# Kernel tuning notes

Hardware: AMD Instinct MI355X
Metric: run time of the kernel (lower is better)

## Reference

```python
import jax, jax.numpy as jnp
import numpy as np

D_IN = 1024
D_OUT = 1024

def setup_inputs() -> dict:
    key = jax.random.key(0)
    kx, kq, kk, kv = jax.random.split(key, 4)
    x = jax.random.normal(kx, (4, 2048, D_IN), dtype=jnp.float32)
    # torch Linear weights are [d_out, d_in]; store as [d_in, d_out] for x @ W
    s = 1.0 / np.sqrt(D_IN)
    Wq = jax.random.uniform(kq, (D_IN, D_OUT), jnp.float32, -s, s)
    Wk = jax.random.uniform(kk, (D_IN, D_OUT), jnp.float32, -s, s)
    Wv = jax.random.uniform(kv, (D_IN, D_OUT), jnp.float32, -s, s)
    return {"x": x, "Wq": Wq, "Wk": Wk, "Wv": Wv}

def reference(x, Wq, Wk, Wv):
    # x: [b, n, d_in]
    n = x.shape[1]
    q = jnp.einsum('bnd,de->bne', x, Wq)
    k = jnp.einsum('bnd,de->bne', x, Wk)
    v = jnp.einsum('bnd,de->bne', x, Wv)
    scores = jnp.einsum('bqe,bke->bqk', q, k)  # [b, n, n]
    causal = jnp.tril(jnp.ones((n, n), dtype=bool))  # True = keep
    scores = jnp.where(causal, scores, -jnp.inf)
    attn = jax.nn.softmax(scores / jnp.sqrt(jnp.float32(k.shape[-1])), axis=-1)
    # dropout p=0.0 -> identity
    return jnp.einsum('bqk,bke->bqe', attn, v)
```

## Files before the change

kernel.cpp:

```cpp
#include <hip/hip_runtime.h>
#include <hip/hip_bf16.h>
#include <stdint.h>

#define D_ 1024
#define NSEQ 2048

typedef __attribute__((ext_vector_type(8))) short bf16x8;
typedef __attribute__((ext_vector_type(4))) float f32x4;

static __device__ __forceinline__ unsigned short f2bf(float x) {
    union { __hip_bfloat16 h; unsigned short u; } cv;
    cv.h = __float2bfloat16(x);
    return cv.u;
}

static __device__ __forceinline__ void gload_lds16(const void* g, void* l) {
    __builtin_amdgcn_global_load_lds(
        (const __attribute__((address_space(1))) unsigned int*)(uintptr_t)g,
        (__attribute__((address_space(3))) unsigned int*)(uintptr_t)l, 16, 0, 0);
}

__global__ __launch_bounds__(256) void cvt_x(const float* __restrict__ x,
                                             __hip_bfloat16* __restrict__ xb) {
    int i = blockIdx.x * 256 + threadIdx.x;
    float4 v = reinterpret_cast<const float4*>(x)[i];
    ushort4 o;
    o.x = f2bf(v.x); o.y = f2bf(v.y); o.z = f2bf(v.z); o.w = f2bf(v.w);
    reinterpret_cast<ushort4*>(xb)[i] = o;
}

__global__ __launch_bounds__(256) void wt_kernel(const float* __restrict__ Wq,
                                                 const float* __restrict__ Wk,
                                                 const float* __restrict__ Wv,
                                                 __hip_bfloat16* __restrict__ Wt) {
    const float* W = (blockIdx.z == 0) ? Wq : (blockIdx.z == 1) ? Wk : Wv;
    unsigned short* O = (unsigned short*)(Wt + (size_t)blockIdx.z * D_ * D_);
    __shared__ float tile[32][33];
    int r0 = blockIdx.y * 32, c0 = blockIdx.x * 32;
    int t = threadIdx.x;
    int r = t >> 3, c4 = (t & 7) * 4;
    float4 v = *reinterpret_cast<const float4*>(&W[(size_t)(r0 + r) * D_ + c0 + c4]);
    tile[r][c4 + 0] = v.x; tile[r][c4 + 1] = v.y;
    tile[r][c4 + 2] = v.z; tile[r][c4 + 3] = v.w;
    __syncthreads();
    int er = t >> 3, dc = (t & 7) * 4;
    ushort4 pk;
    pk.x = f2bf(tile[dc + 0][er]); pk.y = f2bf(tile[dc + 1][er]);
    pk.z = f2bf(tile[dc + 2][er]); pk.w = f2bf(tile[dc + 3][er]);
    *reinterpret_cast<ushort4*>(&O[(size_t)(c0 + er) * D_ + r0 + dc]) = pk;
}

template <int MODE>
__global__ __launch_bounds__(256) void gemm128(const __hip_bfloat16* __restrict__ A, int lda,
                                               const __hip_bfloat16* __restrict__ Bt, int ldb,
                                               void* __restrict__ o0, void* __restrict__ o1,
                                               void* __restrict__ o2,
                                               const float* __restrict__ rinv) {
    const int bx = blockIdx.x, by = blockIdx.y, bz = blockIdx.z;
    if (MODE == 2 && by > bx) return;

    const __hip_bfloat16* Ab = A;
    const __hip_bfloat16* Bb = Bt;
    int Kdim = 1024;
    if (MODE == 2) { Ab += (size_t)bz * NSEQ * D_;  Bb += (size_t)bz * NSEQ * D_; }
    if (MODE == 3) { Ab += (size_t)bz * NSEQ * 4096; Bb += (size_t)bz * D_ * NSEQ; Kdim = (bx + 1) * 128; }

    const int m0 = bx * 128, n0 = by * 128;

    __shared__ __hip_bfloat16 As[128 * 32];
    __shared__ __hip_bfloat16 Bs[128 * 32];

    const int tid = threadIdx.x;
    const int lane = tid & 63, wid = tid >> 6;
    const int wm = wid >> 1, wn = wid & 1;
    const int lr = lane & 15, lk = lane >> 4;

    const int srow = wid * 32 + (lane >> 2);
    const int scol = (lane & 3) * 8;
    const __hip_bfloat16* aptr = Ab + (size_t)(m0 + srow) * lda + scol;
    const __hip_bfloat16* bptr = Bb + (size_t)(n0 + srow) * ldb + scol;
    char* AsW = (char*)As + wid * 2048;
    char* BsW = (char*)Bs + wid * 2048;

    f32x4 acc[4][4] = {};

    for (int k0 = 0; k0 < Kdim; k0 += 32) {
        gload_lds16(aptr,                    AsW);
        gload_lds16(aptr + (size_t)16 * lda, AsW + 1024);
        gload_lds16(bptr,                    BsW);
        gload_lds16(bptr + (size_t)16 * ldb, BsW + 1024);
        aptr += 32; bptr += 32;
        __syncthreads();

        bf16x8 af[4], bfr[4];
#pragma unroll
        for (int m = 0; m < 4; ++m)
            af[m] = *reinterpret_cast<const bf16x8*>(&As[(wm * 64 + m * 16 + lr) * 32 + lk * 8]);
#pragma unroll
        for (int n = 0; n < 4; ++n)
            bfr[n] = *reinterpret_cast<const bf16x8*>(&Bs[(wn * 64 + n * 16 + lr) * 32 + lk * 8]);
#pragma unroll
        for (int m = 0; m < 4; ++m)
#pragma unroll
            for (int n = 0; n < 4; ++n)
                acc[m][n] = __builtin_amdgcn_mfma_f32_16x16x32_bf16(af[m], bfr[n], acc[m][n], 0, 0, 0);
        __syncthreads();
    }

#pragma unroll
    for (int m = 0; m < 4; ++m)
#pragma unroll
        for (int n = 0; n < 4; ++n) {
            const int rbase = m0 + wm * 64 + m * 16 + lk * 4;
            const int cbase = n0 + wn * 64 + n * 16 + lr;
            if (MODE == 0) {
                const int seg = cbase >> 10, e = cbase & 1023;
                if (seg < 2) {
                    unsigned short* C = (unsigned short*)(seg == 0 ? o0 : o1);
#pragma unroll
                    for (int j = 0; j < 4; ++j)
                        C[(size_t)(rbase + j) * D_ + e] = f2bf(acc[m][n][j]);
                } else {
                    unsigned short* Vt = (unsigned short*)o2;
                    const int b = rbase >> 11, nq = rbase & 2047;
                    ushort4 pk;
                    pk.x = f2bf(acc[m][n][0]); pk.y = f2bf(acc[m][n][1]);
                    pk.z = f2bf(acc[m][n][2]); pk.w = f2bf(acc[m][n][3]);
                    *reinterpret_cast<ushort4*>(&Vt[(((size_t)b << 10) + e) * NSEQ + nq]) = pk;
                }
            } else if (MODE == 2) {
                float* S = (float*)o0 + (size_t)bz * NSEQ * NSEQ;
#pragma unroll
                for (int j = 0; j < 4; ++j) {
                    const int qg = rbase + j, kg = cbase;
                    float s = acc[m][n][j] * 0.03125f;
                    if (kg > qg) s = -1e30f;
                    S[(size_t)qg * NSEQ + kg] = s;
                }
            } else if (MODE == 3) {
                float* O = (float*)o0 + (size_t)bz * NSEQ * D_;
#pragma unroll
                for (int j = 0; j < 4; ++j)
                    O[(size_t)(rbase + j) * D_ + cbase] =
                        acc[m][n][j] * rinv[bz * NSEQ + rbase + j];
            }
        }
}

__global__ __launch_bounds__(256) void softmax_rows(float* __restrict__ S,
                                                    float* __restrict__ rinv) {
    int lane = threadIdx.x & 63;
    int row = blockIdx.x * 4 + (threadIdx.x >> 6);
    int q = row & 2047;
    float* srow = S + (size_t)row * NSEQ;
    int L = ((q >> 7) + 1) << 7;

    float mx = -1e30f;
    for (int k = lane * 4; k < L; k += 256) {
        float4 v = *reinterpret_cast<const float4*>(srow + k);
        mx = fmaxf(mx, fmaxf(fmaxf(v.x, v.y), fmaxf(v.z, v.w)));
    }
    for (int off = 32; off > 0; off >>= 1) mx = fmaxf(mx, __shfl_xor(mx, off, 64));

    float sum = 0.f;
    unsigned short* prow = (unsigned short*)srow;
    for (int k = lane * 4; k < L; k += 256) {
        float4 v = *reinterpret_cast<const float4*>(srow + k);
        float e0 = __expf(v.x - mx), e1 = __expf(v.y - mx);
        float e2 = __expf(v.z - mx), e3 = __expf(v.w - mx);
        sum += (e0 + e1) + (e2 + e3);
        ushort4 pk; pk.x = f2bf(e0); pk.y = f2bf(e1); pk.z = f2bf(e2); pk.w = f2bf(e3);
        *reinterpret_cast<ushort4*>(prow + k) = pk;
    }
    for (int off = 32; off > 0; off >>= 1) sum += __shfl_xor(sum, off, 64);
    if (lane == 0) rinv[row] = 1.0f / sum;
}

extern "C" void kernel_launch(void* const* d_in, const int* in_sizes, int n_in,
                              void* d_out, int out_size, void* d_ws, size_t ws_size,
                              hipStream_t stream) {
    const float* x  = (const float*)d_in[0];
    const float* Wq = (const float*)d_in[1];
    const float* Wk = (const float*)d_in[2];
    const float* Wv = (const float*)d_in[3];

    char* ws = (char*)d_ws;
    float*          S    = (float*)(ws);
    __hip_bfloat16* Xb   = (__hip_bfloat16*)(ws + 67108864);
    __hip_bfloat16* Q    = (__hip_bfloat16*)(ws + 83886080);
    __hip_bfloat16* K    = (__hip_bfloat16*)(ws + 100663296);
    __hip_bfloat16* Vt   = (__hip_bfloat16*)(ws + 117440512);
    __hip_bfloat16* Wt   = (__hip_bfloat16*)(ws + 134217728);
    float*          rinv = (float*)(ws + 140509184);

    cvt_x<<<8192, 256, 0, stream>>>(x, Xb);
    wt_kernel<<<dim3(32, 32, 3), 256, 0, stream>>>(Wq, Wk, Wv, Wt);

    gemm128<0><<<dim3(64, 24, 1), 256, 0, stream>>>(Xb, 1024, Wt, 1024, Q, K, Vt, nullptr);
    gemm128<2><<<dim3(16, 16, 4), 256, 0, stream>>>(Q, 1024, K, 1024, S, nullptr, nullptr, nullptr);
    softmax_rows<<<2048, 256, 0, stream>>>(S, rinv);
    gemm128<3><<<dim3(16, 8, 4), 256, 0, stream>>>((const __hip_bfloat16*)S, 4096, Vt, 2048,
                                                   d_out, nullptr, nullptr, rinv);
}
```

Baseline: 193.1 us.

## Replace QKV projection GEMM with 256x256 tile, double-buffered, swizzled LDS pipeline

The fused QKV projection moves from the generic 128x128 single-buffered GEMM to a dedicated 512-thread kernel. It computes 256x256 output tiles and double-buffers a 128 KB LDS region with XOR-swizzled layout. Global-to-LDS loads for the next k-slab are issued while MFMAs run on the current one, using explicit vmcnt waits, barriers and setprio. The aim is to hide global load latency, reduce LDS bank conflicts and raise arithmetic intensity. The cost is heavy LDS use, which limits occupancy, and the 384-block grid may fill the CUs unevenly.

```diff
diff --git a/kernel.cpp b/kernel.cpp
--- a/kernel.cpp
+++ b/kernel.cpp
@@ -50,11 +50,172 @@
     *reinterpret_cast<ushort4*>(&O[(size_t)(c0 + er) * D_ + r0 + dc]) = pk;
 }
 
+
+struct Frags { bf16x8 a0, a1, a2, a3, b0, b1, b2, b3; };
+
+template <int KK, int MH>
+static __device__ __forceinline__ Frags load_frags(const char* bufbase, int aoff, int boff) {
+    const char* regA = bufbase + KK * 16384;
+    const char* regB = bufbase + 32768 + KK * 16384;
+    Frags f;
+    f.a0 = *(const bf16x8*)(regA + aoff + (MH * 4 + 0) * 1024);
+    f.a1 = *(const bf16x8*)(regA + aoff + (MH * 4 + 1) * 1024);
+    f.a2 = *(const bf16x8*)(regA + aoff + (MH * 4 + 2) * 1024);
+    f.a3 = *(const bf16x8*)(regA + aoff + (MH * 4 + 3) * 1024);
+    f.b0 = *(const bf16x8*)(regB + boff + 0);
+    f.b1 = *(const bf16x8*)(regB + boff + 1024);
+    f.b2 = *(const bf16x8*)(regB + boff + 2048);
+    f.b3 = *(const bf16x8*)(regB + boff + 3072);
+    return f;
+}
+
+template <int MH>
+static __device__ __forceinline__ void apply_mfma(const Frags& f, f32x4 (&acc)[8][4]) {
+    acc[MH*4+0][0] = __builtin_amdgcn_mfma_f32_16x16x32_bf16(f.a0, f.b0, acc[MH*4+0][0], 0, 0, 0);
+    acc[MH*4+0][1] = __builtin_amdgcn_mfma_f32_16x16x32_bf16(f.a0, f.b1, acc[MH*4+0][1], 0, 0, 0);
+    acc[MH*4+0][2] = __builtin_amdgcn_mfma_f32_16x16x32_bf16(f.a0, f.b2, acc[MH*4+0][2], 0, 0, 0);
+    acc[MH*4+0][3] = __builtin_amdgcn_mfma_f32_16x16x32_bf16(f.a0, f.b3, acc[MH*4+0][3], 0, 0, 0);
+    acc[MH*4+1][0] = __builtin_amdgcn_mfma_f32_16x16x32_bf16(f.a1, f.b0, acc[MH*4+1][0], 0, 0, 0);
+    acc[MH*4+1][1] = __builtin_amdgcn_mfma_f32_16x16x32_bf16(f.a1, f.b1, acc[MH*4+1][1], 0, 0, 0);
+    acc[MH*4+1][2] = __builtin_amdgcn_mfma_f32_16x16x32_bf16(f.a1, f.b2, acc[MH*4+1][2], 0, 0, 0);
+    acc[MH*4+1][3] = __builtin_amdgcn_mfma_f32_16x16x32_bf16(f.a1, f.b3, acc[MH*4+1][3], 0, 0, 0);
+    acc[MH*4+2][0] = __builtin_amdgcn_mfma_f32_16x16x32_bf16(f.a2, f.b0, acc[MH*4+2][0], 0, 0, 0);
+    acc[MH*4+2][1] = __builtin_amdgcn_mfma_f32_16x16x32_bf16(f.a2, f.b1, acc[MH*4+2][1], 0, 0, 0);
+    acc[MH*4+2][2] = __builtin_amdgcn_mfma_f32_16x16x32_bf16(f.a2, f.b2, acc[MH*4+2][2], 0, 0, 0);
+    acc[MH*4+2][3] = __builtin_amdgcn_mfma_f32_16x16x32_bf16(f.a2, f.b3, acc[MH*4+2][3], 0, 0, 0);
+    acc[MH*4+3][0] = __builtin_amdgcn_mfma_f32_16x16x32_bf16(f.a3, f.b0, acc[MH*4+3][0], 0, 0, 0);
+    acc[MH*4+3][1] = __builtin_amdgcn_mfma_f32_16x16x32_bf16(f.a3, f.b1, acc[MH*4+3][1], 0, 0, 0);
+    acc[MH*4+3][2] = __builtin_amdgcn_mfma_f32_16x16x32_bf16(f.a3, f.b2, acc[MH*4+3][2], 0, 0, 0);
+    acc[MH*4+3][3] = __builtin_amdgcn_mfma_f32_16x16x32_bf16(f.a3, f.b3, acc[MH*4+3][3], 0, 0, 0);
+}
+
+__global__ __launch_bounds__(512, 2) void gemm256_qkv(
+    const __hip_bfloat16* __restrict__ A,
+    const __hip_bfloat16* __restrict__ Bt,
+    void* __restrict__ q_out, void* __restrict__ k_out, void* __restrict__ vt_out) {
+    constexpr int NT = 16;
+    extern __shared__ char lds[];
+
+    const int m0 = blockIdx.x * 256, n0 = blockIdx.y * 256;
+    const int tid = threadIdx.x, lane = tid & 63, wid = tid >> 6;
+    const int wm = wid >> 2, wn = wid & 3;
+    const int lr = lane & 15, lk = lane >> 4;
+
+    const __hip_bfloat16* Apan = A + (size_t)m0 * 1024;
+    const __hip_bfloat16* Bpan = Bt + (size_t)n0 * 1024;
+
+    const int swz = (lk ^ ((lr >> 1) & 3)) << 4;
+    const int aoff = (wm * 128 + lr) * 64 + swz;
+    const int boff = (wn * 64 + lr) * 64 + swz;
+
+    const int sprow = wid * 32 + (lane >> 2);
+    const int sblk = ((lane & 3) ^ ((lane >> 3) & 3)) * 8;
+
+    auto stage = [&](int s) {
+        const int Ts = s >> 2, op = s & 1, kks = (s >> 1) & 1;
+        char* dst = lds + ((Ts & 1) << 16) + (op << 15) + (kks << 14) + (wid << 11);
+        const __hip_bfloat16* g = (op ? Bpan : Apan)
+                                  + (size_t)sprow * 1024 + Ts * 64 + kks * 32 + sblk;
+        gload_lds16(g, dst);
+        gload_lds16(g + (size_t)16 * 1024, dst + 1024);
+    };
+
+    f32x4 acc[8][4] = {};
+
+    stage(0); stage(1); stage(2); stage(3); stage(4);
+    asm volatile("s_waitcnt vmcnt(6)" ::: "memory");
+    __builtin_amdgcn_s_barrier();
+
+    for (int t = 0; t + 2 < NT; ++t) {
+        const char* bb = lds + ((t & 1) << 16);
+        const int s0 = 4 * t + 5;
+        {
+            Frags f = load_frags<0, 0>(bb, aoff, boff);
+            stage(s0 + 0);
+            __builtin_amdgcn_s_barrier();
+            asm volatile("s_waitcnt lgkmcnt(0)" ::: "memory");
+            __builtin_amdgcn_sched_barrier(0);
+            __builtin_amdgcn_s_setprio(1);
+            apply_mfma<0>(f, acc);
+            __builtin_amdgcn_s_setprio(0);
+            __builtin_amdgcn_s_barrier();
+        }
+        {
+            Frags f = load_frags<0, 1>(bb, aoff, boff);
+            stage(s0 + 1);
+            asm volatile("s_waitcnt vmcnt(6)" ::: "memory");
+            __builtin_amdgcn_s_barrier();
+            asm volatile("s_waitcnt lgkmcnt(0)" ::: "memory");
+            __builtin_amdgcn_sched_barrier(0);
+            __builtin_amdgcn_s_setprio(1);
+            apply_mfma<1>(f, acc);
+            __builtin_amdgcn_s_setprio(0);
+            __builtin_amdgcn_s_barrier();
+        }
+        {
+            Frags f = load_frags<1, 0>(bb, aoff, boff);
+            stage(s0 + 2);
+            __builtin_amdgcn_s_barrier();
+            asm volatile("s_waitcnt lgkmcnt(0)" ::: "memory");
+            __builtin_amdgcn_sched_barrier(0);
+            __builtin_amdgcn_s_setprio(1);
+            apply_mfma<0>(f, acc);
+            __builtin_amdgcn_s_setprio(0);
+            __builtin_amdgcn_s_barrier();
+        }
+        {
+            Frags f = load_frags<1, 1>(bb, aoff, boff);
+            stage(s0 + 3);
+            asm volatile("s_waitcnt vmcnt(6)" ::: "memory");
+            __builtin_amdgcn_s_barrier();
+            asm volatile("s_waitcnt lgkmcnt(0)" ::: "memory");
+            __builtin_amdgcn_sched_barrier(0);
+            __builtin_amdgcn_s_setprio(1);
+            apply_mfma<1>(f, acc);
+            __builtin_amdgcn_s_setprio(0);
+            __builtin_amdgcn_s_barrier();
+        }
+    }
+
+    stage(4 * NT - 3); stage(4 * NT - 2); stage(4 * NT - 1);
+    asm volatile("s_waitcnt vmcnt(0)" ::: "memory");
+    __builtin_amdgcn_s_barrier();
+#pragma unroll
+    for (int t = NT - 2; t < NT; ++t) {
+        const char* bb = lds + ((t & 1) << 16);
+        { Frags f = load_frags<0, 0>(bb, aoff, boff); apply_mfma<0>(f, acc); }
+        { Frags f = load_frags<0, 1>(bb, aoff, boff); apply_mfma<1>(f, acc); }
+        { Frags f = load_frags<1, 0>(bb, aoff, boff); apply_mfma<0>(f, acc); }
+        { Frags f = load_frags<1, 1>(bb, aoff, boff); apply_mfma<1>(f, acc); }
+    }
+
+#pragma unroll
+    for (int m = 0; m < 8; ++m)
+#pragma unroll
+        for (int n = 0; n < 4; ++n) {
+            const int rbase = m0 + wm * 128 + m * 16 + lk * 4;
+            const int cbase = n0 + wn * 64 + n * 16 + lr;
+            const int seg = cbase >> 10, e = cbase & 1023;
+            if (seg < 2) {
+                unsigned short* C = (unsigned short*)(seg == 0 ? q_out : k_out);
+#pragma unroll
+                for (int j = 0; j < 4; ++j)
+                    C[(size_t)(rbase + j) * D_ + e] = f2bf(acc[m][n][j]);
+            } else {
+                unsigned short* Vt = (unsigned short*)vt_out;
+                const int b = rbase >> 11, nq = rbase & 2047;
+                ushort4 pk;
+                pk.x = f2bf(acc[m][n][0]); pk.y = f2bf(acc[m][n][1]);
+                pk.z = f2bf(acc[m][n][2]); pk.w = f2bf(acc[m][n][3]);
+                *reinterpret_cast<ushort4*>(&Vt[(((size_t)b << 10) + e) * NSEQ + nq]) = pk;
+            }
+        }
+}
+
 template <int MODE>
 __global__ __launch_bounds__(256) void gemm128(const __hip_bfloat16* __restrict__ A, int lda,
                                                const __hip_bfloat16* __restrict__ Bt, int ldb,
-                                               void* __restrict__ o0, void* __restrict__ o1,
-                                               void* __restrict__ o2,
+                                               void* __restrict__ o0,
                                                const float* __restrict__ rinv) {
     const int bx = blockIdx.x, by = blockIdx.y, bz = blockIdx.z;
     if (MODE == 2 && by > bx) return;
@@ -113,22 +274,7 @@
         for (int n = 0; n < 4; ++n) {
             const int rbase = m0 + wm * 64 + m * 16 + lk * 4;
             const int cbase = n0 + wn * 64 + n * 16 + lr;
-            if (MODE == 0) {
-                const int seg = cbase >> 10, e = cbase & 1023;
-                if (seg < 2) {
-                    unsigned short* C = (unsigned short*)(seg == 0 ? o0 : o1);
-#pragma unroll
-                    for (int j = 0; j < 4; ++j)
-                        C[(size_t)(rbase + j) * D_ + e] = f2bf(acc[m][n][j]);
-                } else {
-                    unsigned short* Vt = (unsigned short*)o2;
-                    const int b = rbase >> 11, nq = rbase & 2047;
-                    ushort4 pk;
-                    pk.x = f2bf(acc[m][n][0]); pk.y = f2bf(acc[m][n][1]);
-                    pk.z = f2bf(acc[m][n][2]); pk.w = f2bf(acc[m][n][3]);
-                    *reinterpret_cast<ushort4*>(&Vt[(((size_t)b << 10) + e) * NSEQ + nq]) = pk;
-                }
-            } else if (MODE == 2) {
+            if (MODE == 2) {
                 float* S = (float*)o0 + (size_t)bz * NSEQ * NSEQ;
 #pragma unroll
                 for (int j = 0; j < 4; ++j) {
@@ -196,9 +342,10 @@
     cvt_x<<<8192, 256, 0, stream>>>(x, Xb);
     wt_kernel<<<dim3(32, 32, 3), 256, 0, stream>>>(Wq, Wk, Wv, Wt);
 
-    gemm128<0><<<dim3(64, 24, 1), 256, 0, stream>>>(Xb, 1024, Wt, 1024, Q, K, Vt, nullptr);
-    gemm128<2><<<dim3(16, 16, 4), 256, 0, stream>>>(Q, 1024, K, 1024, S, nullptr, nullptr, nullptr);
+    gemm256_qkv<<<dim3(32, 12), 512, 131072, stream>>>(Xb, Wt, Q, K, Vt);
+
+    gemm128<2><<<dim3(16, 16, 4), 256, 0, stream>>>(Q, 1024, K, 1024, S, nullptr);
     softmax_rows<<<2048, 256, 0, stream>>>(S, rinv);
     gemm128<3><<<dim3(16, 8, 4), 256, 0, stream>>>((const __hip_bfloat16*)S, 4096, Vt, 2048,
-                                                   d_out, nullptr, nullptr, rinv);
-}
+                                                   d_out, rinv);
+}
```

New measurement: 200.2 us. 3.7% more time.

## Fuse softmax statistics into QK^T epilogue and exponentiate scores inside PV GEMM

Applied to the files above, without the earlier changes.

The QK^T kernel now computes per-64-column partial row max and sum in its epilogue and writes them to small buffers. A tiny merge kernel combines these into the final row max and reciprocal sum. A new PV kernel reads fp32 scores, applies exp and bf16 conversion while staging into LDS, then runs the MFMA loop. This removes the separate softmax pass over the score matrix, but the PV kernel now reads fp32 scores (twice the bytes of bf16) and recomputes exp for each output column tile.

```diff
diff --git a/kernel.cpp b/kernel.cpp
--- a/kernel.cpp
+++ b/kernel.cpp
@@ -54,16 +54,13 @@
 __global__ __launch_bounds__(256) void gemm128(const __hip_bfloat16* __restrict__ A, int lda,
                                                const __hip_bfloat16* __restrict__ Bt, int ldb,
                                                void* __restrict__ o0, void* __restrict__ o1,
-                                               void* __restrict__ o2,
-                                               const float* __restrict__ rinv) {
+                                               void* __restrict__ o2) {
     const int bx = blockIdx.x, by = blockIdx.y, bz = blockIdx.z;
     if (MODE == 2 && by > bx) return;
 
     const __hip_bfloat16* Ab = A;
     const __hip_bfloat16* Bb = Bt;
-    int Kdim = 1024;
     if (MODE == 2) { Ab += (size_t)bz * NSEQ * D_;  Bb += (size_t)bz * NSEQ * D_; }
-    if (MODE == 3) { Ab += (size_t)bz * NSEQ * 4096; Bb += (size_t)bz * D_ * NSEQ; Kdim = (bx + 1) * 128; }
 
     const int m0 = bx * 128, n0 = by * 128;
 
@@ -84,7 +81,7 @@
 
     f32x4 acc[4][4] = {};
 
-    for (int k0 = 0; k0 < Kdim; k0 += 32) {
+    for (int k0 = 0; k0 < 1024; k0 += 32) {
         gload_lds16(aptr,                    AsW);
         gload_lds16(aptr + (size_t)16 * lda, AsW + 1024);
         gload_lds16(bptr,                    BsW);
@@ -107,13 +104,13 @@
         __syncthreads();
     }
 
-#pragma unroll
-    for (int m = 0; m < 4; ++m)
-#pragma unroll
-        for (int n = 0; n < 4; ++n) {
-            const int rbase = m0 + wm * 64 + m * 16 + lk * 4;
-            const int cbase = n0 + wn * 64 + n * 16 + lr;
-            if (MODE == 0) {
+    if (MODE == 0) {
+#pragma unroll
+        for (int m = 0; m < 4; ++m)
+#pragma unroll
+            for (int n = 0; n < 4; ++n) {
+                const int rbase = m0 + wm * 64 + m * 16 + lk * 4;
+                const int cbase = n0 + wn * 64 + n * 16 + lr;
                 const int seg = cbase >> 10, e = cbase & 1023;
                 if (seg < 2) {
                     unsigned short* C = (unsigned short*)(seg == 0 ? o0 : o1);
@@ -128,52 +125,140 @@
                     pk.z = f2bf(acc[m][n][2]); pk.w = f2bf(acc[m][n][3]);
                     *reinterpret_cast<ushort4*>(&Vt[(((size_t)b << 10) + e) * NSEQ + nq]) = pk;
                 }
-            } else if (MODE == 2) {
-                float* S = (float*)o0 + (size_t)bz * NSEQ * NSEQ;
+            }
+    } else {
+        float* S = (float*)o0 + (size_t)bz * NSEQ * NSEQ;
+#pragma unroll
+        for (int m = 0; m < 4; ++m)
+#pragma unroll
+            for (int n = 0; n < 4; ++n) {
+                const int rbase = m0 + wm * 64 + m * 16 + lk * 4;
+                const int cbase = n0 + wn * 64 + n * 16 + lr;
 #pragma unroll
                 for (int j = 0; j < 4; ++j) {
-                    const int qg = rbase + j, kg = cbase;
                     float s = acc[m][n][j] * 0.03125f;
-                    if (kg > qg) s = -1e30f;
-                    S[(size_t)qg * NSEQ + kg] = s;
+                    if (cbase > rbase + j) s = -1e30f;
+                    acc[m][n][j] = s;
+                    S[(size_t)(rbase + j) * NSEQ + cbase] = s;
                 }
-            } else if (MODE == 3) {
-                float* O = (float*)o0 + (size_t)bz * NSEQ * D_;
-#pragma unroll
-                for (int j = 0; j < 4; ++j)
-                    O[(size_t)(rbase + j) * D_ + cbase] =
-                        acc[m][n][j] * rinv[bz * NSEQ + rbase + j];
             }
+        float* Pm = (float*)o1;
+        float* Pl = (float*)o2;
+        const int pcol = by * 2 + wn;
+#pragma unroll
+        for (int m = 0; m < 4; ++m)
+#pragma unroll
+            for (int j = 0; j < 4; ++j) {
+                float mx = fmaxf(fmaxf(acc[m][0][j], acc[m][1][j]),
+                                 fmaxf(acc[m][2][j], acc[m][3][j]));
+#pragma unroll
+                for (int w = 1; w < 16; w <<= 1) mx = fmaxf(mx, __shfl_xor(mx, w, 64));
+                float sm = __expf(acc[m][0][j] - mx) + __expf(acc[m][1][j] - mx) +
+                           __expf(acc[m][2][j] - mx) + __expf(acc[m][3][j] - mx);
+#pragma unroll
+                for (int w = 1; w < 16; w <<= 1) sm += __shfl_xor(sm, w, 64);
+                if (lr == 0) {
+                    const int row = bz * NSEQ + m0 + wm * 64 + m * 16 + lk * 4 + j;
+                    Pm[row * 32 + pcol] = mx;
+                    Pl[row * 32 + pcol] = sm;
+                }
+            }
+    }
+}
+
+__global__ __launch_bounds__(256) void merge_stats(const float* __restrict__ Pm,
+                                                   const float* __restrict__ Pl,
+                                                   float2* __restrict__ rl) {
+    int row = blockIdx.x * 256 + threadIdx.x;
+    int q = row & 2047;
+    int nc = 2 * ((q >> 7) + 1);
+    float m = -3e38f, l = 0.f;
+    for (int c = 0; c < nc; ++c) {
+        float mb = Pm[row * 32 + c], lb = Pl[row * 32 + c];
+        float nm = fmaxf(m, mb);
+        l = l * __expf(m - nm) + lb * __expf(mb - nm);
+        m = nm;
+    }
+    rl[row] = make_float2(m, 1.0f / l);
+}
+
+__global__ __launch_bounds__(256) void pv128(const float* __restrict__ S,
+                                             const __hip_bfloat16* __restrict__ Vt,
+                                             const float2* __restrict__ rl,
+                                             float* __restrict__ Out) {
+    const int bx = blockIdx.x, by = blockIdx.y, bz = blockIdx.z;
+    const float* Sb = S + (size_t)bz * NSEQ * NSEQ;
+    const __hip_bfloat16* Bb = Vt + (size_t)bz * D_ * NSEQ;
+    const int Kdim = (bx + 1) * 128;
+    const int m0 = bx * 128, n0 = by * 128;
+
+    __shared__ unsigned short Ap[128][40];
+    __shared__ __hip_bfloat16 Bs[128 * 32];
+
+    const int tid = threadIdx.x;
+    const int lane = tid & 63, wid = tid >> 6;
+    const int wm = wid >> 1, wn = wid & 1;
+    const int lr = lane & 15, lk = lane >> 4;
+
+    const int ar = tid >> 1, ah = (tid & 1) * 16;
+    const float mrow = rl[bz * NSEQ + m0 + ar].x;
+    const float* srow = Sb + (size_t)(m0 + ar) * NSEQ + ah;
+
+    const int srB = wid * 32 + (lane >> 2);
+    const int scB = (lane & 3) * 8;
+    const __hip_bfloat16* bptr = Bb + (size_t)(n0 + srB) * NSEQ + scB;
+    char* BsW = (char*)Bs + wid * 2048;
+
+    f32x4 acc[4][4] = {};
+
+    for (int k0 = 0; k0 < Kdim; k0 += 32) {
+        gload_lds16(bptr,                     BsW);
+        gload_lds16(bptr + (size_t)16 * NSEQ, BsW + 1024);
+        bptr += 32;
+        float4 v0 = *reinterpret_cast<const float4*>(srow + k0 + 0);
+        float4 v1 = *reinterpret_cast<const float4*>(srow + k0 + 4);
+        float4 v2 = *reinterpret_cast<const float4*>(srow + k0 + 8);
+        float4 v3 = *reinterpret_cast<const float4*>(srow + k0 + 12);
+        union { unsigned short u[8]; uint4 v; } p0, p1;
+        p0.u[0] = f2bf(__expf(v0.x - mrow)); p0.u[1] = f2bf(__expf(v0.y - mrow));
+        p0.u[2] = f2bf(__expf(v0.z - mrow)); p0.u[3] = f2bf(__expf(v0.w - mrow));
+        p0.u[4] = f2bf(__expf(v1.x - mrow)); p0.u[5] = f2bf(__expf(v1.y - mrow));
+        p0.u[6] = f2bf(__expf(v1.z - mrow)); p0.u[7] = f2bf(__expf(v1.w - mrow));
+        p1.u[0] = f2bf(__expf(v2.x - mrow)); p1.u[1] = f2bf(__expf(v2.y - mrow));
+        p1.u[2] = f2bf(__expf(v2.z - mrow)); p1.u[3] = f2bf(__expf(v2.w - mrow));
+        p1.u[4] = f2bf(__expf(v3.x - mrow)); p1.u[5] = f2bf(__expf(v3.y - mrow));
+        p1.u[6] = f2bf(__expf(v3.z - mrow)); p1.u[7] = f2bf(__expf(v3.w - mrow));
+        *reinterpret_cast<uint4*>(&Ap[ar][ah + 0]) = p0.v;
+        *reinterpret_cast<uint4*>(&Ap[ar][ah + 8]) = p1.v;
+        __syncthreads();
+
+        bf16x8 af[4], bfr[4];
+#pragma unroll
+        for (int m = 0; m < 4; ++m)
+            af[m] = *reinterpret_cast<const bf16x8*>(&Ap[wm * 64 + m * 16 + lr][lk * 8]);
+#pragma unroll
+        for (int n = 0; n < 4; ++n)
+            bfr[n] = *reinterpret_cast<const bf16x8*>(&Bs[(wn * 64 + n * 16 + lr) * 32 + lk * 8]);
+#pragma unroll
+        for (int m = 0; m < 4; ++m)
+#pragma unroll
+            for (int n = 0; n < 4; ++n)
+                acc[m][n] = __builtin_amdgcn_mfma_f32_16x16x32_bf16(af[m], bfr[n], acc[m][n], 0, 0, 0);
+        __syncthreads();
+    }
+
+    float* O = Out + (size_t)bz * NSEQ * D_;
+#pragma unroll
+    for (int m = 0; m < 4; ++m)
+#pragma unroll
+        for (int n = 0; n < 4; ++n) {
+            const int rbase = m0 + wm * 64 + m * 16 + lk * 4;
+            const int cbase = n0 + wn * 64 + n * 16 + lr;
+#pragma unroll
+            for (int j = 0; j < 4; ++j)
+                O[(size_t)(rbase + j) * D_ + cbase] =
+                    acc[m][n][j] * rl[bz * NSEQ + rbase + j].y;
         }
-}
-
-__global__ __launch_bounds__(256) void softmax_rows(float* __restrict__ S,
-                                                    float* __restrict__ rinv) {
-    int lane = threadIdx.x & 63;
-    int row = blockIdx.x * 4 + (threadIdx.x >> 6);
-    int q = row & 2047;
-    float* srow = S + (size_t)row * NSEQ;
-    int L = ((q >> 7) + 1) << 7;
-
-    float mx = -1e30f;
-    for (int k = lane * 4; k < L; k += 256) {
-        float4 v = *reinterpret_cast<const float4*>(srow + k);
-        mx = fmaxf(mx, fmaxf(fmaxf(v.x, v.y), fmaxf(v.z, v.w)));
-    }
-    for (int off = 32; off > 0; off >>= 1) mx = fmaxf(mx, __shfl_xor(mx, off, 64));
-
-    float sum = 0.f;
-    unsigned short* prow = (unsigned short*)srow;
-    for (int k = lane * 4; k < L; k += 256) {
-        float4 v = *reinterpret_cast<const float4*>(srow + k);
-        float e0 = __expf(v.x - mx), e1 = __expf(v.y - mx);
-        float e2 = __expf(v.z - mx), e3 = __expf(v.w - mx);
-        sum += (e0 + e1) + (e2 + e3);
-        ushort4 pk; pk.x = f2bf(e0); pk.y = f2bf(e1); pk.z = f2bf(e2); pk.w = f2bf(e3);
-        *reinterpret_cast<ushort4*>(prow + k) = pk;
-    }
-    for (int off = 32; off > 0; off >>= 1) sum += __shfl_xor(sum, off, 64);
-    if (lane == 0) rinv[row] = 1.0f / sum;
 }
 
 extern "C" void kernel_launch(void* const* d_in, const int* in_sizes, int n_in,
@@ -191,14 +276,16 @@
     __hip_bfloat16* K    = (__hip_bfloat16*)(ws + 100663296);
     __hip_bfloat16* Vt   = (__hip_bfloat16*)(ws + 117440512);
     __hip_bfloat16* Wt   = (__hip_bfloat16*)(ws + 134217728);
-    float*          rinv = (float*)(ws + 140509184);
+    float*  Pm = (float*)(ws + 67108864);
+    float*  Pl = (float*)(ws + 68157440);
+    float2* rl = (float2*)(ws + 69206016);
 
     cvt_x<<<8192, 256, 0, stream>>>(x, Xb);
     wt_kernel<<<dim3(32, 32, 3), 256, 0, stream>>>(Wq, Wk, Wv, Wt);
 
-    gemm128<0><<<dim3(64, 24, 1), 256, 0, stream>>>(Xb, 1024, Wt, 1024, Q, K, Vt, nullptr);
-    gemm128<2><<<dim3(16, 16, 4), 256, 0, stream>>>(Q, 1024, K, 1024, S, nullptr, nullptr, nullptr);
-    softmax_rows<<<2048, 256, 0, stream>>>(S, rinv);
-    gemm128<3><<<dim3(16, 8, 4), 256, 0, stream>>>((const __hip_bfloat16*)S, 4096, Vt, 2048,
-                                                   d_out, nullptr, nullptr, rinv);
-}
+    gemm128<0><<<dim3(64, 24, 1), 256, 0, stream>>>(Xb, 1024, Wt, 1024, Q, K, Vt);
+
+    gemm128<2><<<dim3(16, 16, 4), 256, 0, stream>>>(Q, 1024, K, 1024, S, Pm, Pl);
+    merge_stats<<<32, 256, 0, stream>>>(Pm, Pl, rl);
+    pv128<<<dim3(16, 8, 4), 256, 0, stream>>>(S, Vt, rl, (float*)d_out);
+}
```

New measurement: 219.5 us. 1.14x slower.

## Compute partial softmax max/sum in QK GEMM epilogue, single-pass finish kernel

Applied to the files above, without the earlier changes.

The QK^T GEMM epilogue now computes per-row max and exp-sum over each wave's 64-column slice and writes these partial statistics to workspace. A new softmax_finish kernel merges the partials with an online-softmax rescale, then makes one pass over S to write bf16 exponentials, replacing the old two-pass read of the score rows. The goal is to cut one full read of the large fp32 score matrix. In exchange the GEMM epilogue does extra exp and shuffle work, and the Pm/Pl buffers reuse the Xb workspace region, which is already consumed by then.

```diff
diff --git a/kernel.cpp b/kernel.cpp
--- a/kernel.cpp
+++ b/kernel.cpp
@@ -55,7 +55,7 @@
                                                const __hip_bfloat16* __restrict__ Bt, int ldb,
                                                void* __restrict__ o0, void* __restrict__ o1,
                                                void* __restrict__ o2,
-                                               const float* __restrict__ rinv) {
+                                               const float2* __restrict__ rl) {
     const int bx = blockIdx.x, by = blockIdx.y, bz = blockIdx.z;
     if (MODE == 2 && by > bx) return;
 
@@ -107,13 +107,13 @@
         __syncthreads();
     }
 
-#pragma unroll
-    for (int m = 0; m < 4; ++m)
-#pragma unroll
-        for (int n = 0; n < 4; ++n) {
-            const int rbase = m0 + wm * 64 + m * 16 + lk * 4;
-            const int cbase = n0 + wn * 64 + n * 16 + lr;
-            if (MODE == 0) {
+    if (MODE == 0) {
+#pragma unroll
+        for (int m = 0; m < 4; ++m)
+#pragma unroll
+            for (int n = 0; n < 4; ++n) {
+                const int rbase = m0 + wm * 64 + m * 16 + lk * 4;
+                const int cbase = n0 + wn * 64 + n * 16 + lr;
                 const int seg = cbase >> 10, e = cbase & 1023;
                 if (seg < 2) {
                     unsigned short* C = (unsigned short*)(seg == 0 ? o0 : o1);
@@ -128,52 +128,89 @@
                     pk.z = f2bf(acc[m][n][2]); pk.w = f2bf(acc[m][n][3]);
                     *reinterpret_cast<ushort4*>(&Vt[(((size_t)b << 10) + e) * NSEQ + nq]) = pk;
                 }
-            } else if (MODE == 2) {
-                float* S = (float*)o0 + (size_t)bz * NSEQ * NSEQ;
+            }
+    } else if (MODE == 2) {
+        float* S = (float*)o0 + (size_t)bz * NSEQ * NSEQ;
+#pragma unroll
+        for (int m = 0; m < 4; ++m)
+#pragma unroll
+            for (int n = 0; n < 4; ++n) {
+                const int rbase = m0 + wm * 64 + m * 16 + lk * 4;
+                const int cbase = n0 + wn * 64 + n * 16 + lr;
 #pragma unroll
                 for (int j = 0; j < 4; ++j) {
-                    const int qg = rbase + j, kg = cbase;
                     float s = acc[m][n][j] * 0.03125f;
-                    if (kg > qg) s = -1e30f;
-                    S[(size_t)qg * NSEQ + kg] = s;
+                    if (cbase > rbase + j) s = -1e30f;
+                    acc[m][n][j] = s;
+                    S[(size_t)(rbase + j) * NSEQ + cbase] = s;
                 }
-            } else if (MODE == 3) {
-                float* O = (float*)o0 + (size_t)bz * NSEQ * D_;
+            }
+        float* Pm = (float*)o1;
+        float* Pl = (float*)o2;
+        const int pcol = by * 2 + wn;
+#pragma unroll
+        for (int m = 0; m < 4; ++m)
+#pragma unroll
+            for (int j = 0; j < 4; ++j) {
+                float mx = fmaxf(fmaxf(acc[m][0][j], acc[m][1][j]),
+                                 fmaxf(acc[m][2][j], acc[m][3][j]));
+#pragma unroll
+                for (int w = 1; w < 16; w <<= 1) mx = fmaxf(mx, __shfl_xor(mx, w, 64));
+                float sm = __expf(acc[m][0][j] - mx) + __expf(acc[m][1][j] - mx) +
+                           __expf(acc[m][2][j] - mx) + __expf(acc[m][3][j] - mx);
+#pragma unroll
+                for (int w = 1; w < 16; w <<= 1) sm += __shfl_xor(sm, w, 64);
+                if (lr == 0) {
+                    const int row = bz * NSEQ + m0 + wm * 64 + m * 16 + lk * 4 + j;
+                    Pm[row * 32 + pcol] = mx;
+                    Pl[row * 32 + pcol] = sm;
+                }
+            }
+    } else {
+        float* O = (float*)o0 + (size_t)bz * NSEQ * D_;
+#pragma unroll
+        for (int m = 0; m < 4; ++m)
+#pragma unroll
+            for (int n = 0; n < 4; ++n) {
+                const int rbase = m0 + wm * 64 + m * 16 + lk * 4;
+                const int cbase = n0 + wn * 64 + n * 16 + lr;
 #pragma unroll
                 for (int j = 0; j < 4; ++j)
                     O[(size_t)(rbase + j) * D_ + cbase] =
-                        acc[m][n][j] * rinv[bz * NSEQ + rbase + j];
-            }
-        }
-}
-
-__global__ __launch_bounds__(256) void softmax_rows(float* __restrict__ S,
-                                                    float* __restrict__ rinv) {
-    int lane = threadIdx.x & 63;
-    int row = blockIdx.x * 4 + (threadIdx.x >> 6);
-    int q = row & 2047;
+                        acc[m][n][j] * rl[bz * NSEQ + rbase + j].y;
+            }
+    }
+}
+
+__global__ __launch_bounds__(256) void softmax_finish(float* __restrict__ S,
+                                                      const float* __restrict__ Pm,
+                                                      const float* __restrict__ Pl,
+                                                      float2* __restrict__ rl) {
+    const int lane = threadIdx.x & 63;
+    const int row = blockIdx.x * 4 + (threadIdx.x >> 6);
+    const int q = row & 2047;
+    const int nb = (q >> 7) + 1;
+    const int nc = nb * 2;
+
+    float mb = (lane < nc) ? Pm[row * 32 + lane] : -3e38f;
+    float m = mb;
+#pragma unroll
+    for (int off = 32; off > 0; off >>= 1) m = fmaxf(m, __shfl_xor(m, off, 64));
+    float lb = (lane < nc) ? Pl[row * 32 + lane] * __expf(mb - m) : 0.f;
+#pragma unroll
+    for (int off = 32; off > 0; off >>= 1) lb += __shfl_xor(lb, off, 64);
+    if (lane == 0) rl[row] = make_float2(m, 1.0f / lb);
+
     float* srow = S + (size_t)row * NSEQ;
-    int L = ((q >> 7) + 1) << 7;
-
-    float mx = -1e30f;
+    unsigned short* prow = (unsigned short*)srow;
+    const int L = nb << 7;
     for (int k = lane * 4; k < L; k += 256) {
         float4 v = *reinterpret_cast<const float4*>(srow + k);
-        mx = fmaxf(mx, fmaxf(fmaxf(v.x, v.y), fmaxf(v.z, v.w)));
-    }
-    for (int off = 32; off > 0; off >>= 1) mx = fmaxf(mx, __shfl_xor(mx, off, 64));
-
-    float sum = 0.f;
-    unsigned short* prow = (unsigned short*)srow;
-    for (int k = lane * 4; k < L; k += 256) {
-        float4 v = *reinterpret_cast<const float4*>(srow + k);
-        float e0 = __expf(v.x - mx), e1 = __expf(v.y - mx);
-        float e2 = __expf(v.z - mx), e3 = __expf(v.w - mx);
-        sum += (e0 + e1) + (e2 + e3);
-        ushort4 pk; pk.x = f2bf(e0); pk.y = f2bf(e1); pk.z = f2bf(e2); pk.w = f2bf(e3);
+        ushort4 pk;
+        pk.x = f2bf(__expf(v.x - m)); pk.y = f2bf(__expf(v.y - m));
+        pk.z = f2bf(__expf(v.z - m)); pk.w = f2bf(__expf(v.w - m));
         *reinterpret_cast<ushort4*>(prow + k) = pk;
     }
-    for (int off = 32; off > 0; off >>= 1) sum += __shfl_xor(sum, off, 64);
-    if (lane == 0) rinv[row] = 1.0f / sum;
 }
 
 extern "C" void kernel_launch(void* const* d_in, const int* in_sizes, int n_in,
@@ -191,14 +228,17 @@
     __hip_bfloat16* K    = (__hip_bfloat16*)(ws + 100663296);
     __hip_bfloat16* Vt   = (__hip_bfloat16*)(ws + 117440512);
     __hip_bfloat16* Wt   = (__hip_bfloat16*)(ws + 134217728);
-    float*          rinv = (float*)(ws + 140509184);
+    float*  Pm = (float*)(ws + 67108864);
+    float*  Pl = (float*)(ws + 68157440);
+    float2* rl = (float2*)(ws + 69206016);
 
     cvt_x<<<8192, 256, 0, stream>>>(x, Xb);
     wt_kernel<<<dim3(32, 32, 3), 256, 0, stream>>>(Wq, Wk, Wv, Wt);
 
     gemm128<0><<<dim3(64, 24, 1), 256, 0, stream>>>(Xb, 1024, Wt, 1024, Q, K, Vt, nullptr);
-    gemm128<2><<<dim3(16, 16, 4), 256, 0, stream>>>(Q, 1024, K, 1024, S, nullptr, nullptr, nullptr);
-    softmax_rows<<<2048, 256, 0, stream>>>(S, rinv);
+
+    gemm128<2><<<dim3(16, 16, 4), 256, 0, stream>>>(Q, 1024, K, 1024, S, Pm, Pl, nullptr);
+    softmax_finish<<<2048, 256, 0, stream>>>(S, Pm, Pl, rl);
     gemm128<3><<<dim3(16, 8, 4), 256, 0, stream>>>((const __hip_bfloat16*)S, 4096, Vt, 2048,
-                                                   d_out, nullptr, nullptr, rinv);
-}
+                                                   d_out, nullptr, nullptr, rl);
+}
```

Measured after the change: 202.4 us. 4.8% more time.
